# Kernel optimization log

Hardware: AMD Instinct MI355X
Metric: run time of the kernel (lower is better)

Reference implementation:

```python
import jax, jax.numpy as jnp
import numpy as np

EPS = 1e-5  # BatchNorm eps


def _conv(x, w, pad):
    # NCHW / OIHW stride-1 convolution (matches nn.Conv2d(..., padding=pad, bias=False))
    return jax.lax.conv_general_dilated(
        x, w, window_strides=(1, 1), padding=[(pad, pad), (pad, pad)],
        dimension_numbers=("NCHW", "OIHW", "NCHW"))


def _bn2d(x, g, b, m, v):
    # inference-mode BN folded to a per-channel affine
    s = g * jax.lax.rsqrt(v + EPS)
    return x * s[None, :, None, None] + (b - m * s)[None, :, None, None]


def _pool2(x):
    # AvgPool2d(2): non-overlapping 2x2 mean
    n, c, h, w = x.shape
    return x.reshape(n, c, h // 2, 2, w // 2, 2).mean(axis=(3, 5))


def _block(x, w, g, b, m, v):
    # Conv -> BN -> ReLU -> AvgPool2 -> Hardtanh(0,1)
    x = _conv(x, w, pad=2)
    x = _bn2d(x, g, b, m, v)
    x = jax.nn.relu(x)
    x = _pool2(x)
    return jnp.clip(x, 0.0, 1.0)


def setup_inputs() -> dict:
    key = jax.random.key(0)
    ks = jax.random.split(key, 24)
    B = 1024
    x = jax.random.uniform(ks[0], (B, 3, 32, 32), dtype=jnp.float32)

    def wgt(k, shape):
        fan_in = shape[1] * shape[2] * shape[3]
        return jax.random.normal(k, shape, jnp.float32) / np.float32(np.sqrt(fan_in))

    def bn(k, c):
        k1, k2, k3, k4 = jax.random.split(k, 4)
        g = jax.random.uniform(k1, (c,), jnp.float32, 0.5, 1.5)
        b = jax.random.normal(k2, (c,), jnp.float32) * 0.1
        m = jax.random.normal(k3, (c,), jnp.float32) * 0.1
        v = jax.random.uniform(k4, (c,), jnp.float32, 0.5, 1.5)
        return g, b, m, v

    w1 = wgt(ks[1], (32, 3, 5, 5))
    w2 = wgt(ks[2], (32, 32, 5, 5))
    w3 = wgt(ks[3], (64, 32, 5, 5))
    w4 = wgt(ks[4], (10, 64, 4, 4))  # fc1 as a 4x4 valid conv
    g1, b1, m1, v1 = bn(ks[5], 32)
    g2, b2, m2, v2 = bn(ks[6], 32)
    g3, b3, m3, v3 = bn(ks[7], 64)
    g4, b4, m4, v4 = bn(ks[8], 10)
    return dict(x=x,
                w1=w1, g1=g1, b1=b1, m1=m1, v1=v1,
                w2=w2, g2=g2, b2=b2, m2=m2, v2=v2,
                w3=w3, g3=g3, b3=b3, m3=m3, v3=v3,
                w4=w4, g4=g4, b4=b4, m4=m4, v4=v4)


def reference(x,
              w1, g1, b1, m1, v1,
              w2, g2, b2, m2, v2,
              w3, g3, b3, m3, v3,
              w4, g4, b4, m4, v4):
    x = _block(x, w1, g1, b1, m1, v1)   # [B,32,16,16]
    x = _block(x, w2, g2, b2, m2, v2)   # [B,32,8,8]
    x = _block(x, w3, g3, b3, m3, v3)   # [B,64,4,4]
    x = _conv(x, w4, pad=0)             # [B,10,1,1]
    x = x.reshape(x.shape[0], -1)       # flatten -> [B,10]
    s = g4 * jax.lax.rsqrt(v4 + EPS)    # BatchNorm1d_fixed (inference affine)
    return x * s[None, :] + (b4 - m4 * s)[None, :]
```

## Files before the change

kernel.cpp:

```cpp
#include <hip/hip_runtime.h>
#include <hip/hip_bf16.h>

#define EPS 1e-5f

typedef __bf16 v8bf __attribute__((ext_vector_type(8)));
typedef __bf16 v4bf __attribute__((ext_vector_type(4)));
typedef float  v4f  __attribute__((ext_vector_type(4)));

__global__ void k_wtrans(const float* __restrict__ w1, const float* __restrict__ w2,
                         const float* __restrict__ w3,
                         __hip_bfloat16* __restrict__ fb1, __hip_bfloat16* __restrict__ fb2,
                         __hip_bfloat16* __restrict__ fb3)
{
    int idx = blockIdx.x * 256 + threadIdx.x;
    if (idx < 640) {
        int lane = idx & 63, fi = idx >> 6;
        int ky = fi >> 1, nt = fi & 1;
        int oc = nt * 16 + (lane & 15), k0 = (lane >> 4) * 8;
        __hip_bfloat16* dst = fb1 + idx * 8;
        #pragma unroll
        for (int j = 0; j < 8; ++j) {
            int k = k0 + j, dx = k >> 2, ic = k & 3;
            float val = (dx < 5 && ic < 3) ? w1[oc * 75 + ic * 25 + ky * 5 + dx] : 0.f;
            dst[j] = __float2bfloat16(val);
        }
    } else if (idx < 640 + 3200) {
        int k2 = idx - 640;
        int lane = k2 & 63, fi = k2 >> 6;
        int tap = fi >> 1, nt = fi & 1;
        int oc = nt * 16 + (lane & 15), ic0 = (lane >> 4) * 8;
        __hip_bfloat16* dst = fb2 + k2 * 8;
        #pragma unroll
        for (int j = 0; j < 8; ++j)
            dst[j] = __float2bfloat16(w2[oc * 800 + (ic0 + j) * 25 + tap]);
    } else if (idx < 640 + 3200 + 6400) {
        int k3 = idx - 3840;
        int lane = k3 & 63, fi = k3 >> 6;
        int tap = fi >> 2, nt = fi & 3;
        int oc = nt * 16 + (lane & 15), ic0 = (lane >> 4) * 8;
        __hip_bfloat16* dst = fb3 + k3 * 8;
        #pragma unroll
        for (int j = 0; j < 8; ++j)
            dst[j] = __float2bfloat16(w3[oc * 800 + (ic0 + j) * 25 + tap]);
    }
}

#define XS2(row, col, blk) ((__hip_bfloat16*)(pool + (((((row)*20 + (col))*32) + (((blk) ^ ((col)&3))*8))*2)))
#define XS2S(row, col, oc) ((__hip_bfloat16*)(pool + (((((row)*20 + (col))*32) + ((((oc)>>3) ^ ((col)&3))*8) + ((oc)&7))*2)))
#define XS1(row, col)      ((__hip_bfloat16*)(pool + 25600 + ((((row)*39 + (col))*4)*2)))
#define XS3(row, col, blk) ((__hip_bfloat16*)(pool + 25600 + (((((row)*12 + (col))*32) + (((blk) ^ ((col)&3))*8))*2)))
#define XS3S(row, col, oc) ((__hip_bfloat16*)(pool + 25600 + (((((row)*12 + (col))*32) + ((((oc)>>3) ^ ((col)&3))*8) + ((oc)&7))*2)))

__global__ __launch_bounds__(512, 4) void k_fused(
    const float* __restrict__ x,
    const __hip_bfloat16* __restrict__ fb1,
    const __hip_bfloat16* __restrict__ fb2,
    const __hip_bfloat16* __restrict__ fb3,
    const float* __restrict__ w4,
    const float* __restrict__ g1, const float* __restrict__ b1,
    const float* __restrict__ m1, const float* __restrict__ v1,
    const float* __restrict__ g2, const float* __restrict__ b2,
    const float* __restrict__ m2, const float* __restrict__ v2,
    const float* __restrict__ g3, const float* __restrict__ b3,
    const float* __restrict__ m3, const float* __restrict__ v3,
    const float* __restrict__ g4, const float* __restrict__ b4,
    const float* __restrict__ m4, const float* __restrict__ v4,
    float* __restrict__ out)
{
    __shared__ __align__(16) unsigned char pool[36832];
    __shared__ float sc1[32], bi1[32], sc2[32], bi2[32], sc3[64], bi3[64];
    float* fin = (float*)pool;

    const int img = blockIdx.x, t = threadIdx.x;
    const int lane = t & 63, wave = t >> 6;
    const int lo = lane & 15, hi = lane >> 4;

    for (int i = t; i < 2302; i += 512) ((uint4*)pool)[i] = make_uint4(0, 0, 0, 0);
    if (t < 32) {
        float s = g1[t] * rsqrtf(v1[t] + EPS); sc1[t] = s; bi1[t] = b1[t] - m1[t] * s;
        float u = g2[t] * rsqrtf(v2[t] + EPS); sc2[t] = u; bi2[t] = b2[t] - m2[t] * u;
    }
    if (t < 64) {
        float s = g3[t] * rsqrtf(v3[t] + EPS); sc3[t] = s; bi3[t] = b3[t] - m3[t] * s;
    }
    __syncthreads();

    for (int i = t; i < 768; i += 512) {
        float4 val = *(const float4*)(x + (size_t)img * 3072 + i * 4);
        int ic = i >> 8, rem = i & 255;
        int y = rem >> 3, xx = (rem & 7) * 4;
        XS1(y + 2, xx + 2)[ic] = __float2bfloat16(val.x);
        XS1(y + 2, xx + 3)[ic] = __float2bfloat16(val.y);
        XS1(y + 2, xx + 4)[ic] = __float2bfloat16(val.z);
        XS1(y + 2, xx + 5)[ic] = __float2bfloat16(val.w);
    }
    __syncthreads();

    {
        const int y0 = 4 * wave;
        #pragma unroll
        for (int xh = 0; xh < 2; ++xh) {
            const int xx = xh * 16 + lo + hi * 2;
            v8bf av[8];
            #pragma unroll
            for (int r = 0; r < 8; ++r) {
                v4bf lo4 = *(const v4bf*)XS1(y0 + r, xx);
                v4bf hi4 = *(const v4bf*)XS1(y0 + r, xx + 1);
                av[r] = __builtin_shufflevector(lo4, hi4, 0, 1, 2, 3, 4, 5, 6, 7);
            }
            #pragma unroll
            for (int nt = 0; nt < 2; ++nt) {
                v8bf bw[5];
                #pragma unroll
                for (int ky = 0; ky < 5; ++ky)
                    bw[ky] = *(const v8bf*)(fb1 + ((ky * 2 + nt) * 64 + lane) * 8);
                v4f acc[2][2];
                #pragma unroll
                for (int a0 = 0; a0 < 2; ++a0)
                    #pragma unroll
                    for (int a1 = 0; a1 < 2; ++a1)
                        acc[a0][a1] = (v4f){0.f, 0.f, 0.f, 0.f};
                #pragma unroll
                for (int ky = 0; ky < 5; ++ky) {
                    acc[0][0] = __builtin_amdgcn_mfma_f32_16x16x32_bf16(av[ky],     bw[ky], acc[0][0], 0, 0, 0);
                    acc[0][1] = __builtin_amdgcn_mfma_f32_16x16x32_bf16(av[ky + 1], bw[ky], acc[0][1], 0, 0, 0);
                    acc[1][0] = __builtin_amdgcn_mfma_f32_16x16x32_bf16(av[ky + 2], bw[ky], acc[1][0], 0, 0, 0);
                    acc[1][1] = __builtin_amdgcn_mfma_f32_16x16x32_bf16(av[ky + 3], bw[ky], acc[1][1], 0, 0, 0);
                }
                const int oc = nt * 16 + lo;
                const float s = sc1[oc], bb = bi1[oc];
                #pragma unroll
                for (int pri = 0; pri < 2; ++pri) {
                    float u0 = fmaxf(fmaf(acc[pri][0][0], s, bb), 0.f);
                    float u1 = fmaxf(fmaf(acc[pri][0][1], s, bb), 0.f);
                    float u2 = fmaxf(fmaf(acc[pri][0][2], s, bb), 0.f);
                    float u3 = fmaxf(fmaf(acc[pri][0][3], s, bb), 0.f);
                    float q0 = fmaxf(fmaf(acc[pri][1][0], s, bb), 0.f);
                    float q1 = fmaxf(fmaf(acc[pri][1][1], s, bb), 0.f);
                    float q2 = fmaxf(fmaf(acc[pri][1][2], s, bb), 0.f);
                    float q3 = fmaxf(fmaf(acc[pri][1][3], s, bb), 0.f);
                    float p0 = fminf(0.25f * (u0 + u1 + q0 + q1), 1.f);
                    float p1 = fminf(0.25f * (u2 + u3 + q2 + q3), 1.f);
                    const int pr = 2 * wave + pri;
                    const int px = xh * 8 + hi * 2;
                    *XS2S(pr + 2, px + 2, oc) = __float2bfloat16(p0);
                    *XS2S(pr + 2, px + 3, oc) = __float2bfloat16(p1);
                }
            }
        }
    }
    __syncthreads();

    {
        uint* x3u = (uint*)(pool + 25600);
        for (int i = t; i < 1280; i += 512) {
            int u;
            if (i < 384)      u = i;
            else if (i < 768) u = 1920 + (i - 384);
            else {
                int j = i - 768;
                int r = 2 + (j >> 6), c = j & 63;
                u = r * 192 + (c < 32 ? c : 128 + c);
            }
            x3u[u] = 0u;
        }

        const int nt = wave & 1, wgrp = wave >> 1;
        v4f acc[2][2];
        #pragma unroll
        for (int a0 = 0; a0 < 2; ++a0)
            #pragma unroll
            for (int a1 = 0; a1 < 2; ++a1)
                acc[a0][a1] = (v4f){0.f, 0.f, 0.f, 0.f};

        #pragma unroll
        for (int kx = 0; kx < 5; ++kx) {
            v8bf bf[5];
            #pragma unroll
            for (int ky = 0; ky < 5; ++ky)
                bf[ky] = *(const v8bf*)(fb2 + ((ky * 5 + kx) * 2 + nt) * 512 + lane * 8);
            v8bf av[8];
            #pragma unroll
            for (int r = 0; r < 8; ++r)
                av[r] = *(const v8bf*)XS2(4 * wgrp + r, lo + kx, hi);
            #pragma unroll
            for (int ky = 0; ky < 5; ++ky) {
                acc[0][0] = __builtin_amdgcn_mfma_f32_16x16x32_bf16(av[ky],     bf[ky], acc[0][0], 0, 0, 0);
                acc[0][1] = __builtin_amdgcn_mfma_f32_16x16x32_bf16(av[ky + 1], bf[ky], acc[0][1], 0, 0, 0);
                acc[1][0] = __builtin_amdgcn_mfma_f32_16x16x32_bf16(av[ky + 2], bf[ky], acc[1][0], 0, 0, 0);
                acc[1][1] = __builtin_amdgcn_mfma_f32_16x16x32_bf16(av[ky + 3], bf[ky], acc[1][1], 0, 0, 0);
            }
        }

        const int oc = nt * 16 + lo;
        const float s = sc2[oc], bb = bi2[oc];
        #pragma unroll
        for (int pri = 0; pri < 2; ++pri) {
            const int rp = wgrp * 2 + pri;
            float u0 = fmaxf(fmaf(acc[pri][0][0], s, bb), 0.f);
            float u1 = fmaxf(fmaf(acc[pri][0][1], s, bb), 0.f);
            float u2 = fmaxf(fmaf(acc[pri][0][2], s, bb), 0.f);
            float u3 = fmaxf(fmaf(acc[pri][0][3], s, bb), 0.f);
            float q0 = fmaxf(fmaf(acc[pri][1][0], s, bb), 0.f);
            float q1 = fmaxf(fmaf(acc[pri][1][1], s, bb), 0.f);
            float q2 = fmaxf(fmaf(acc[pri][1][2], s, bb), 0.f);
            float q3 = fmaxf(fmaf(acc[pri][1][3], s, bb), 0.f);
            float p0 = fminf(0.25f * (u0 + u1 + q0 + q1), 1.f);
            float p1 = fminf(0.25f * (u2 + u3 + q2 + q3), 1.f);
            *XS3S(rp + 2, hi * 2 + 2, oc) = __float2bfloat16(p0);
            *XS3S(rp + 2, hi * 2 + 3, oc) = __float2bfloat16(p1);
        }
    }
    __syncthreads();

    {
        const int nt = wave >> 1, mh = wave & 1;
        const int oc = nt * 16 + lo;
        const int ya0 = lo >> 3, xa = lo & 7;
        v4f acc[2];
        #pragma unroll
        for (int q = 0; q < 2; ++q) acc[q] = (v4f){0.f, 0.f, 0.f, 0.f};

        #pragma unroll
        for (int ky = 0; ky < 5; ++ky) {
            v8bf bf[5];
            #pragma unroll
            for (int kx = 0; kx < 5; ++kx)
                bf[kx] = *(const v8bf*)(fb3 + ((ky * 5 + kx) * 4 + nt) * 512 + lane * 8);
            #pragma unroll
            for (int kx = 0; kx < 5; ++kx) {
                #pragma unroll
                for (int mi = 0; mi < 2; ++mi) {
                    const int mt = mh * 2 + mi;
                    v8bf av = *(const v8bf*)XS3(2 * mt + ya0 + ky, xa + kx, hi);
                    acc[mi] = __builtin_amdgcn_mfma_f32_16x16x32_bf16(av, bf[kx], acc[mi], 0, 0, 0);
                }
            }
        }

        const float s = sc3[oc], bb = bi3[oc];
        const int xb = (hi & 1) * 2;
        #pragma unroll
        for (int mi = 0; mi < 2; ++mi) {
            const int mt = mh * 2 + mi;
            float v0 = fmaxf(fmaf(acc[mi][0], s, bb), 0.f);
            float v1 = fmaxf(fmaf(acc[mi][1], s, bb), 0.f);
            float v2 = fmaxf(fmaf(acc[mi][2], s, bb), 0.f);
            float v3 = fmaxf(fmaf(acc[mi][3], s, bb), 0.f);
            float s01 = v0 + v1, s23 = v2 + v3;
            float o01 = __shfl_xor(s01, 32);
            float o23 = __shfl_xor(s23, 32);
            float p0 = fminf(0.25f * (s01 + o01), 1.f);
            float p1 = fminf(0.25f * (s23 + o23), 1.f);
            if (hi < 2) {
                fin[oc * 16 + mt * 4 + xb]     = p0;
                fin[oc * 16 + mt * 4 + xb + 1] = p1;
            }
        }
    }
    __syncthreads();

    {
        for (int oc = wave; oc < 10; oc += 8) {
            const float4* wp = (const float4*)(w4 + oc * 1024);
            const float4* fp = (const float4*)fin;
            float acc0 = 0.f, acc1 = 0.f;
            #pragma unroll
            for (int ch = 0; ch < 4; ++ch) {
                float4 a = fp[ch * 64 + lane];
                float4 w = wp[ch * 64 + lane];
                acc0 = fmaf(a.x, w.x, acc0); acc1 = fmaf(a.y, w.y, acc1);
                acc0 = fmaf(a.z, w.z, acc0); acc1 = fmaf(a.w, w.w, acc1);
            }
            float acc = acc0 + acc1;
            acc += __shfl_xor(acc, 1);
            acc += __shfl_xor(acc, 2);
            acc += __shfl_xor(acc, 4);
            acc += __shfl_xor(acc, 8);
            acc += __shfl_xor(acc, 16);
            acc += __shfl_xor(acc, 32);
            if (lane == 0) {
                float s = g4[oc] * rsqrtf(v4[oc] + EPS);
                out[img * 10 + oc] = acc * s + (b4[oc] - m4[oc] * s);
            }
        }
    }
}

extern "C" void kernel_launch(void* const* d_in, const int* in_sizes, int n_in,
                              void* d_out, int out_size, void* d_ws, size_t ws_size,
                              hipStream_t stream) {
    const float* x  = (const float*)d_in[0];
    const float* w1 = (const float*)d_in[1];
    const float* g1 = (const float*)d_in[2];
    const float* b1 = (const float*)d_in[3];
    const float* m1 = (const float*)d_in[4];
    const float* v1 = (const float*)d_in[5];
    const float* w2 = (const float*)d_in[6];
    const float* g2 = (const float*)d_in[7];
    const float* b2 = (const float*)d_in[8];
    const float* m2 = (const float*)d_in[9];
    const float* v2 = (const float*)d_in[10];
    const float* w3 = (const float*)d_in[11];
    const float* g3 = (const float*)d_in[12];
    const float* b3 = (const float*)d_in[13];
    const float* m3 = (const float*)d_in[14];
    const float* v3 = (const float*)d_in[15];
    const float* w4 = (const float*)d_in[16];
    const float* g4 = (const float*)d_in[17];
    const float* b4 = (const float*)d_in[18];
    const float* m4 = (const float*)d_in[19];
    const float* v4 = (const float*)d_in[20];
    float* out = (float*)d_out;

    char* base = (char*)d_ws;
    __hip_bfloat16* fb1 = (__hip_bfloat16*)base;
    __hip_bfloat16* fb2 = (__hip_bfloat16*)(base + 16384);
    __hip_bfloat16* fb3 = (__hip_bfloat16*)(base + 67584);

    k_wtrans<<<40, 256, 0, stream>>>(w1, w2, w3, fb1, fb2, fb3);
    k_fused<<<1024, 512, 0, stream>>>(x, fb1, fb2, fb3, w4,
                                      g1, b1, m1, v1, g2, b2, m2, v2,
                                      g3, b3, m3, v3, g4, b4, m4, v4, out);
}
```

Before: 40.00 us.

## Rework conv2/conv3 wave tiling, stronger LDS swizzle, border-only zeroing, packed input load

In conv2, each wave now owns one pooled output row and both output-channel tiles, so each A fragment feeds two MFMAs and fewer redundant A rows are loaded per wave. In conv3, each wave owns one M tile and two N tiles, loading A once per tap and streaming B directly. The LDS swizzle adds a second XOR term to reduce bank conflicts. Full LDS zeroing is replaced by zeroing only the padding borders, and the input is written as packed 3-channel bf16 cells with one barrier removed. The trade-off is more B-fragment registers in conv2 and more complex index arithmetic.

```diff
diff --git a/kernel.cpp b/kernel.cpp
--- a/kernel.cpp
+++ b/kernel.cpp
@@ -45,11 +45,12 @@
     }
 }
 
-#define XS2(row, col, blk) ((__hip_bfloat16*)(pool + (((((row)*20 + (col))*32) + (((blk) ^ ((col)&3))*8))*2)))
-#define XS2S(row, col, oc) ((__hip_bfloat16*)(pool + (((((row)*20 + (col))*32) + ((((oc)>>3) ^ ((col)&3))*8) + ((oc)&7))*2)))
+#define SWZ(blk, col)      ((blk) ^ ((col) & 3) ^ (((col) >> 2) & 3))
+#define XS2(row, col, blk) ((__hip_bfloat16*)(pool + (((((row)*20 + (col))*32) + (SWZ(blk,col)*8))*2)))
+#define XS2S(row, col, oc) ((__hip_bfloat16*)(pool + (((((row)*20 + (col))*32) + (SWZ((oc)>>3,col)*8) + ((oc)&7))*2)))
 #define XS1(row, col)      ((__hip_bfloat16*)(pool + 25600 + ((((row)*39 + (col))*4)*2)))
-#define XS3(row, col, blk) ((__hip_bfloat16*)(pool + 25600 + (((((row)*12 + (col))*32) + (((blk) ^ ((col)&3))*8))*2)))
-#define XS3S(row, col, oc) ((__hip_bfloat16*)(pool + 25600 + (((((row)*12 + (col))*32) + ((((oc)>>3) ^ ((col)&3))*8) + ((oc)&7))*2)))
+#define XS3(row, col, blk) ((__hip_bfloat16*)(pool + 25600 + (((((row)*12 + (col))*32) + (SWZ(blk,col)*8))*2)))
+#define XS3S(row, col, oc) ((__hip_bfloat16*)(pool + 25600 + (((((row)*12 + (col))*32) + (SWZ((oc)>>3,col)*8) + ((oc)&7))*2)))
 
 __global__ __launch_bounds__(512, 4) void k_fused(
     const float* __restrict__ x,
@@ -75,7 +76,6 @@
     const int lane = t & 63, wave = t >> 6;
     const int lo = lane & 15, hi = lane >> 4;
 
-    for (int i = t; i < 2302; i += 512) ((uint4*)pool)[i] = make_uint4(0, 0, 0, 0);
     if (t < 32) {
         float s = g1[t] * rsqrtf(v1[t] + EPS); sc1[t] = s; bi1[t] = b1[t] - m1[t] * s;
         float u = g2[t] * rsqrtf(v2[t] + EPS); sc2[t] = u; bi2[t] = b2[t] - m2[t] * u;
@@ -83,16 +83,31 @@
     if (t < 64) {
         float s = g3[t] * rsqrtf(v3[t] + EPS); sc3[t] = s; bi3[t] = b3[t] - m3[t] * s;
     }
-    __syncthreads();
-
-    for (int i = t; i < 768; i += 512) {
-        float4 val = *(const float4*)(x + (size_t)img * 3072 + i * 4);
-        int ic = i >> 8, rem = i & 255;
-        int y = rem >> 3, xx = (rem & 7) * 4;
-        XS1(y + 2, xx + 2)[ic] = __float2bfloat16(val.x);
-        XS1(y + 2, xx + 3)[ic] = __float2bfloat16(val.y);
-        XS1(y + 2, xx + 4)[ic] = __float2bfloat16(val.z);
-        XS1(y + 2, xx + 5)[ic] = __float2bfloat16(val.w);
+    for (int i = t; i < 956; i += 512) {
+        if (i < 380) {
+            int row, col;
+            if (i < 156) { int rr = i / 39; row = rr < 2 ? rr : rr + 32; col = i % 39; }
+            else { int j = i - 156; row = 2 + j / 7; int cc = j % 7; col = cc < 2 ? cc : cc + 32; }
+            *(uint2*)(pool + 25600 + (row * 39 + col) * 8) = make_uint2(0u, 0u);
+        } else {
+            int k = i - 380;
+            int cell = k >> 2, q = k & 3;
+            int row, col;
+            if (cell < 80) { int rr = cell / 20; row = rr < 2 ? rr : rr + 16; col = cell % 20; }
+            else { int j = cell - 80; row = 2 + (j >> 2); int c2 = j & 3; col = c2 < 2 ? c2 : c2 + 16; }
+            *(uint4*)(pool + ((row * 20 + col) * 32 + q * 8) * 2) = make_uint4(0u, 0u, 0u, 0u);
+        }
+    }
+    for (int c = t; c < 1024; c += 512) {
+        int y = c >> 5, xx = c & 31;
+        int base = img * 3072 + (y << 5) + xx;
+        float f0 = x[base], f1 = x[base + 1024], f2 = x[base + 2048];
+        __hip_bfloat16 h0 = __float2bfloat16(f0);
+        __hip_bfloat16 h1 = __float2bfloat16(f1);
+        __hip_bfloat16 h2 = __float2bfloat16(f2);
+        uint lo32 = (uint)*(unsigned short*)&h0 | ((uint)*(unsigned short*)&h1 << 16);
+        uint hi32 = (uint)*(unsigned short*)&h2;
+        *(uint2*)XS1(y + 2, xx + 2) = make_uint2(lo32, hi32);
     }
     __syncthreads();
 
@@ -165,7 +180,7 @@
             x3u[u] = 0u;
         }
 
-        const int nt = wave & 1, wgrp = wave >> 1;
+        const int rp = wave;
         v4f acc[2][2];
         #pragma unroll
         for (int a0 = 0; a0 < 2; ++a0)
@@ -175,36 +190,37 @@
 
         #pragma unroll
         for (int kx = 0; kx < 5; ++kx) {
-            v8bf bf[5];
+            v8bf bf[5][2];
             #pragma unroll
             for (int ky = 0; ky < 5; ++ky)
-                bf[ky] = *(const v8bf*)(fb2 + ((ky * 5 + kx) * 2 + nt) * 512 + lane * 8);
-            v8bf av[8];
-            #pragma unroll
-            for (int r = 0; r < 8; ++r)
-                av[r] = *(const v8bf*)XS2(4 * wgrp + r, lo + kx, hi);
+                #pragma unroll
+                for (int nt = 0; nt < 2; ++nt)
+                    bf[ky][nt] = *(const v8bf*)(fb2 + ((ky * 5 + kx) * 2 + nt) * 512 + lane * 8);
+            v8bf av[6];
+            #pragma unroll
+            for (int r = 0; r < 6; ++r)
+                av[r] = *(const v8bf*)XS2(2 * rp + r, lo + kx, hi);
             #pragma unroll
             for (int ky = 0; ky < 5; ++ky) {
-                acc[0][0] = __builtin_amdgcn_mfma_f32_16x16x32_bf16(av[ky],     bf[ky], acc[0][0], 0, 0, 0);
-                acc[0][1] = __builtin_amdgcn_mfma_f32_16x16x32_bf16(av[ky + 1], bf[ky], acc[0][1], 0, 0, 0);
-                acc[1][0] = __builtin_amdgcn_mfma_f32_16x16x32_bf16(av[ky + 2], bf[ky], acc[1][0], 0, 0, 0);
-                acc[1][1] = __builtin_amdgcn_mfma_f32_16x16x32_bf16(av[ky + 3], bf[ky], acc[1][1], 0, 0, 0);
-            }
-        }
-
-        const int oc = nt * 16 + lo;
-        const float s = sc2[oc], bb = bi2[oc];
-        #pragma unroll
-        for (int pri = 0; pri < 2; ++pri) {
-            const int rp = wgrp * 2 + pri;
-            float u0 = fmaxf(fmaf(acc[pri][0][0], s, bb), 0.f);
-            float u1 = fmaxf(fmaf(acc[pri][0][1], s, bb), 0.f);
-            float u2 = fmaxf(fmaf(acc[pri][0][2], s, bb), 0.f);
-            float u3 = fmaxf(fmaf(acc[pri][0][3], s, bb), 0.f);
-            float q0 = fmaxf(fmaf(acc[pri][1][0], s, bb), 0.f);
-            float q1 = fmaxf(fmaf(acc[pri][1][1], s, bb), 0.f);
-            float q2 = fmaxf(fmaf(acc[pri][1][2], s, bb), 0.f);
-            float q3 = fmaxf(fmaf(acc[pri][1][3], s, bb), 0.f);
+                acc[0][0] = __builtin_amdgcn_mfma_f32_16x16x32_bf16(av[ky],     bf[ky][0], acc[0][0], 0, 0, 0);
+                acc[0][1] = __builtin_amdgcn_mfma_f32_16x16x32_bf16(av[ky],     bf[ky][1], acc[0][1], 0, 0, 0);
+                acc[1][0] = __builtin_amdgcn_mfma_f32_16x16x32_bf16(av[ky + 1], bf[ky][0], acc[1][0], 0, 0, 0);
+                acc[1][1] = __builtin_amdgcn_mfma_f32_16x16x32_bf16(av[ky + 1], bf[ky][1], acc[1][1], 0, 0, 0);
+            }
+        }
+
+        #pragma unroll
+        for (int nt = 0; nt < 2; ++nt) {
+            const int oc = nt * 16 + lo;
+            const float s = sc2[oc], bb = bi2[oc];
+            float u0 = fmaxf(fmaf(acc[0][nt][0], s, bb), 0.f);
+            float u1 = fmaxf(fmaf(acc[0][nt][1], s, bb), 0.f);
+            float u2 = fmaxf(fmaf(acc[0][nt][2], s, bb), 0.f);
+            float u3 = fmaxf(fmaf(acc[0][nt][3], s, bb), 0.f);
+            float q0 = fmaxf(fmaf(acc[1][nt][0], s, bb), 0.f);
+            float q1 = fmaxf(fmaf(acc[1][nt][1], s, bb), 0.f);
+            float q2 = fmaxf(fmaf(acc[1][nt][2], s, bb), 0.f);
+            float q3 = fmaxf(fmaf(acc[1][nt][3], s, bb), 0.f);
             float p0 = fminf(0.25f * (u0 + u1 + q0 + q1), 1.f);
             float p1 = fminf(0.25f * (u2 + u3 + q2 + q3), 1.f);
             *XS3S(rp + 2, hi * 2 + 2, oc) = __float2bfloat16(p0);
@@ -214,39 +230,33 @@
     __syncthreads();
 
     {
-        const int nt = wave >> 1, mh = wave & 1;
-        const int oc = nt * 16 + lo;
+        const int mt = wave >> 1, nh = wave & 1;
         const int ya0 = lo >> 3, xa = lo & 7;
         v4f acc[2];
         #pragma unroll
         for (int q = 0; q < 2; ++q) acc[q] = (v4f){0.f, 0.f, 0.f, 0.f};
 
         #pragma unroll
-        for (int ky = 0; ky < 5; ++ky) {
-            v8bf bf[5];
-            #pragma unroll
-            for (int kx = 0; kx < 5; ++kx)
-                bf[kx] = *(const v8bf*)(fb3 + ((ky * 5 + kx) * 4 + nt) * 512 + lane * 8);
+        for (int ky = 0; ky < 5; ++ky)
             #pragma unroll
             for (int kx = 0; kx < 5; ++kx) {
-                #pragma unroll
-                for (int mi = 0; mi < 2; ++mi) {
-                    const int mt = mh * 2 + mi;
-                    v8bf av = *(const v8bf*)XS3(2 * mt + ya0 + ky, xa + kx, hi);
-                    acc[mi] = __builtin_amdgcn_mfma_f32_16x16x32_bf16(av, bf[kx], acc[mi], 0, 0, 0);
-                }
-            }
-        }
-
-        const float s = sc3[oc], bb = bi3[oc];
+                const int tap = ky * 5 + kx;
+                v8bf av = *(const v8bf*)XS3(2 * mt + ya0 + ky, xa + kx, hi);
+                v8bf b0 = *(const v8bf*)(fb3 + (tap * 4 + nh * 2 + 0) * 512 + lane * 8);
+                v8bf b1 = *(const v8bf*)(fb3 + (tap * 4 + nh * 2 + 1) * 512 + lane * 8);
+                acc[0] = __builtin_amdgcn_mfma_f32_16x16x32_bf16(av, b0, acc[0], 0, 0, 0);
+                acc[1] = __builtin_amdgcn_mfma_f32_16x16x32_bf16(av, b1, acc[1], 0, 0, 0);
+            }
+
         const int xb = (hi & 1) * 2;
         #pragma unroll
-        for (int mi = 0; mi < 2; ++mi) {
-            const int mt = mh * 2 + mi;
-            float v0 = fmaxf(fmaf(acc[mi][0], s, bb), 0.f);
-            float v1 = fmaxf(fmaf(acc[mi][1], s, bb), 0.f);
-            float v2 = fmaxf(fmaf(acc[mi][2], s, bb), 0.f);
-            float v3 = fmaxf(fmaf(acc[mi][3], s, bb), 0.f);
+        for (int ni = 0; ni < 2; ++ni) {
+            const int oc = (nh * 2 + ni) * 16 + lo;
+            const float s = sc3[oc], bb = bi3[oc];
+            float v0 = fmaxf(fmaf(acc[ni][0], s, bb), 0.f);
+            float v1 = fmaxf(fmaf(acc[ni][1], s, bb), 0.f);
+            float v2 = fmaxf(fmaf(acc[ni][2], s, bb), 0.f);
+            float v3 = fmaxf(fmaf(acc[ni][3], s, bb), 0.f);
             float s01 = v0 + v1, s23 = v2 + v3;
             float o01 = __shfl_xor(s01, 32);
             float o23 = __shfl_xor(s23, 32);
```

New measurement: 47.48 us. 18.7% more time.

## Process two images per block to reuse conv weight fragments

Applied to the files above, without the earlier changes.

Each workgroup now handles two images, with duplicated LDS buffers for both. Weight fragments loaded for conv1/conv2/conv3 are shared across the two images' MFMA sequences. Conv3's wave tiling is restructured so each wave covers two output-channel tiles for both images. This cuts global weight loads and per-block setup at the cost of doubled LDS, more accumulator registers and half as many blocks.

```diff
diff --git a/kernel.cpp b/kernel.cpp
--- a/kernel.cpp
+++ b/kernel.cpp
@@ -45,11 +45,12 @@
     }
 }
 
-#define XS2(row, col, blk) ((__hip_bfloat16*)(pool + (((((row)*20 + (col))*32) + (((blk) ^ ((col)&3))*8))*2)))
-#define XS2S(row, col, oc) ((__hip_bfloat16*)(pool + (((((row)*20 + (col))*32) + ((((oc)>>3) ^ ((col)&3))*8) + ((oc)&7))*2)))
-#define XS1(row, col)      ((__hip_bfloat16*)(pool + 25600 + ((((row)*39 + (col))*4)*2)))
-#define XS3(row, col, blk) ((__hip_bfloat16*)(pool + 25600 + (((((row)*12 + (col))*32) + (((blk) ^ ((col)&3))*8))*2)))
-#define XS3S(row, col, oc) ((__hip_bfloat16*)(pool + 25600 + (((((row)*12 + (col))*32) + ((((oc)>>3) ^ ((col)&3))*8) + ((oc)&7))*2)))
+#define SWZ(blk, col)          ((blk) ^ ((col) & 3))
+#define XS2(im, row, col, blk) ((__hip_bfloat16*)(pool + (im)*25600 + (((((row)*20 + (col))*32) + (SWZ(blk,col)*8))*2)))
+#define XS2S(im, row, col, oc) ((__hip_bfloat16*)(pool + (im)*25600 + (((((row)*20 + (col))*32) + (SWZ((oc)>>3,col)*8) + ((oc)&7))*2)))
+#define XS1(im, row, col)      ((__hip_bfloat16*)(pool + 51200 + (im)*11232 + ((((row)*39 + (col))*4)*2)))
+#define XS3(im, row, col, blk) ((__hip_bfloat16*)(pool + 51200 + (im)*9216 + (((((row)*12 + (col))*32) + (SWZ(blk,col)*8))*2)))
+#define XS3S(im, row, col, oc) ((__hip_bfloat16*)(pool + 51200 + (im)*9216 + (((((row)*12 + (col))*32) + (SWZ((oc)>>3,col)*8) + ((oc)&7))*2)))
 
 __global__ __launch_bounds__(512, 4) void k_fused(
     const float* __restrict__ x,
@@ -67,15 +68,14 @@
     const float* __restrict__ m4, const float* __restrict__ v4,
     float* __restrict__ out)
 {
-    __shared__ __align__(16) unsigned char pool[36832];
+    __shared__ __align__(16) unsigned char pool[73664];
     __shared__ float sc1[32], bi1[32], sc2[32], bi2[32], sc3[64], bi3[64];
-    float* fin = (float*)pool;
-
-    const int img = blockIdx.x, t = threadIdx.x;
+
+    const int img0 = blockIdx.x * 2, t = threadIdx.x;
     const int lane = t & 63, wave = t >> 6;
     const int lo = lane & 15, hi = lane >> 4;
 
-    for (int i = t; i < 2302; i += 512) ((uint4*)pool)[i] = make_uint4(0, 0, 0, 0);
+    for (int i = t; i < 4604; i += 512) ((uint4*)pool)[i] = make_uint4(0, 0, 0, 0);
     if (t < 32) {
         float s = g1[t] * rsqrtf(v1[t] + EPS); sc1[t] = s; bi1[t] = b1[t] - m1[t] * s;
         float u = g2[t] * rsqrtf(v2[t] + EPS); sc2[t] = u; bi2[t] = b2[t] - m2[t] * u;
@@ -85,66 +85,75 @@
     }
     __syncthreads();
 
-    for (int i = t; i < 768; i += 512) {
-        float4 val = *(const float4*)(x + (size_t)img * 3072 + i * 4);
-        int ic = i >> 8, rem = i & 255;
-        int y = rem >> 3, xx = (rem & 7) * 4;
-        XS1(y + 2, xx + 2)[ic] = __float2bfloat16(val.x);
-        XS1(y + 2, xx + 3)[ic] = __float2bfloat16(val.y);
-        XS1(y + 2, xx + 4)[ic] = __float2bfloat16(val.z);
-        XS1(y + 2, xx + 5)[ic] = __float2bfloat16(val.w);
+    #pragma unroll
+    for (int im = 0; im < 2; ++im) {
+        for (int i = t; i < 768; i += 512) {
+            float4 val = *(const float4*)(x + (size_t)(img0 + im) * 3072 + i * 4);
+            int ic = i >> 8, rem = i & 255;
+            int y = rem >> 3, xx = (rem & 7) * 4;
+            XS1(im, y + 2, xx + 2)[ic] = __float2bfloat16(val.x);
+            XS1(im, y + 2, xx + 3)[ic] = __float2bfloat16(val.y);
+            XS1(im, y + 2, xx + 4)[ic] = __float2bfloat16(val.z);
+            XS1(im, y + 2, xx + 5)[ic] = __float2bfloat16(val.w);
+        }
     }
     __syncthreads();
 
     {
+        v8bf bw[5][2];
+        #pragma unroll
+        for (int ky = 0; ky < 5; ++ky)
+            #pragma unroll
+            for (int nt = 0; nt < 2; ++nt)
+                bw[ky][nt] = *(const v8bf*)(fb1 + ((ky * 2 + nt) * 64 + lane) * 8);
+
         const int y0 = 4 * wave;
         #pragma unroll
-        for (int xh = 0; xh < 2; ++xh) {
-            const int xx = xh * 16 + lo + hi * 2;
-            v8bf av[8];
-            #pragma unroll
-            for (int r = 0; r < 8; ++r) {
-                v4bf lo4 = *(const v4bf*)XS1(y0 + r, xx);
-                v4bf hi4 = *(const v4bf*)XS1(y0 + r, xx + 1);
-                av[r] = __builtin_shufflevector(lo4, hi4, 0, 1, 2, 3, 4, 5, 6, 7);
-            }
-            #pragma unroll
-            for (int nt = 0; nt < 2; ++nt) {
-                v8bf bw[5];
-                #pragma unroll
-                for (int ky = 0; ky < 5; ++ky)
-                    bw[ky] = *(const v8bf*)(fb1 + ((ky * 2 + nt) * 64 + lane) * 8);
-                v4f acc[2][2];
-                #pragma unroll
-                for (int a0 = 0; a0 < 2; ++a0)
+        for (int im = 0; im < 2; ++im) {
+            #pragma unroll
+            for (int xh = 0; xh < 2; ++xh) {
+                const int xx = xh * 16 + lo + hi * 2;
+                v8bf av[8];
+                #pragma unroll
+                for (int r = 0; r < 8; ++r) {
+                    v4bf lo4 = *(const v4bf*)XS1(im, y0 + r, xx);
+                    v4bf hi4 = *(const v4bf*)XS1(im, y0 + r, xx + 1);
+                    av[r] = __builtin_shufflevector(lo4, hi4, 0, 1, 2, 3, 4, 5, 6, 7);
+                }
+                #pragma unroll
+                for (int nt = 0; nt < 2; ++nt) {
+                    v4f acc[2][2];
                     #pragma unroll
-                    for (int a1 = 0; a1 < 2; ++a1)
-                        acc[a0][a1] = (v4f){0.f, 0.f, 0.f, 0.f};
-                #pragma unroll
-                for (int ky = 0; ky < 5; ++ky) {
-                    acc[0][0] = __builtin_amdgcn_mfma_f32_16x16x32_bf16(av[ky],     bw[ky], acc[0][0], 0, 0, 0);
-                    acc[0][1] = __builtin_amdgcn_mfma_f32_16x16x32_bf16(av[ky + 1], bw[ky], acc[0][1], 0, 0, 0);
-                    acc[1][0] = __builtin_amdgcn_mfma_f32_16x16x32_bf16(av[ky + 2], bw[ky], acc[1][0], 0, 0, 0);
-                    acc[1][1] = __builtin_amdgcn_mfma_f32_16x16x32_bf16(av[ky + 3], bw[ky], acc[1][1], 0, 0, 0);
-                }
-                const int oc = nt * 16 + lo;
-                const float s = sc1[oc], bb = bi1[oc];
-                #pragma unroll
-                for (int pri = 0; pri < 2; ++pri) {
-                    float u0 = fmaxf(fmaf(acc[pri][0][0], s, bb), 0.f);
-                    float u1 = fmaxf(fmaf(acc[pri][0][1], s, bb), 0.f);
-                    float u2 = fmaxf(fmaf(acc[pri][0][2], s, bb), 0.f);
-                    float u3 = fmaxf(fmaf(acc[pri][0][3], s, bb), 0.f);
-                    float q0 = fmaxf(fmaf(acc[pri][1][0], s, bb), 0.f);
-                    float q1 = fmaxf(fmaf(acc[pri][1][1], s, bb), 0.f);
-                    float q2 = fmaxf(fmaf(acc[pri][1][2], s, bb), 0.f);
-                    float q3 = fmaxf(fmaf(acc[pri][1][3], s, bb), 0.f);
-                    float p0 = fminf(0.25f * (u0 + u1 + q0 + q1), 1.f);
-                    float p1 = fminf(0.25f * (u2 + u3 + q2 + q3), 1.f);
-                    const int pr = 2 * wave + pri;
-                    const int px = xh * 8 + hi * 2;
-                    *XS2S(pr + 2, px + 2, oc) = __float2bfloat16(p0);
-                    *XS2S(pr + 2, px + 3, oc) = __float2bfloat16(p1);
+                    for (int a0 = 0; a0 < 2; ++a0)
+                        #pragma unroll
+                        for (int a1 = 0; a1 < 2; ++a1)
+                            acc[a0][a1] = (v4f){0.f, 0.f, 0.f, 0.f};
+                    #pragma unroll
+                    for (int ky = 0; ky < 5; ++ky) {
+                        acc[0][0] = __builtin_amdgcn_mfma_f32_16x16x32_bf16(av[ky],     bw[ky][nt], acc[0][0], 0, 0, 0);
+                        acc[0][1] = __builtin_amdgcn_mfma_f32_16x16x32_bf16(av[ky + 1], bw[ky][nt], acc[0][1], 0, 0, 0);
+                        acc[1][0] = __builtin_amdgcn_mfma_f32_16x16x32_bf16(av[ky + 2], bw[ky][nt], acc[1][0], 0, 0, 0);
+                        acc[1][1] = __builtin_amdgcn_mfma_f32_16x16x32_bf16(av[ky + 3], bw[ky][nt], acc[1][1], 0, 0, 0);
+                    }
+                    const int oc = nt * 16 + lo;
+                    const float s = sc1[oc], bb = bi1[oc];
+                    #pragma unroll
+                    for (int pri = 0; pri < 2; ++pri) {
+                        float u0 = fmaxf(fmaf(acc[pri][0][0], s, bb), 0.f);
+                        float u1 = fmaxf(fmaf(acc[pri][0][1], s, bb), 0.f);
+                        float u2 = fmaxf(fmaf(acc[pri][0][2], s, bb), 0.f);
+                        float u3 = fmaxf(fmaf(acc[pri][0][3], s, bb), 0.f);
+                        float q0 = fmaxf(fmaf(acc[pri][1][0], s, bb), 0.f);
+                        float q1 = fmaxf(fmaf(acc[pri][1][1], s, bb), 0.f);
+                        float q2 = fmaxf(fmaf(acc[pri][1][2], s, bb), 0.f);
+                        float q3 = fmaxf(fmaf(acc[pri][1][3], s, bb), 0.f);
+                        float p0 = fminf(0.25f * (u0 + u1 + q0 + q1), 1.f);
+                        float p1 = fminf(0.25f * (u2 + u3 + q2 + q3), 1.f);
+                        const int pr = 2 * wave + pri;
+                        const int px = xh * 8 + hi * 2;
+                        *XS2S(im, pr + 2, px + 2, oc) = __float2bfloat16(p0);
+                        *XS2S(im, pr + 2, px + 3, oc) = __float2bfloat16(p1);
+                    }
                 }
             }
         }
@@ -152,26 +161,29 @@
     __syncthreads();
 
     {
-        uint* x3u = (uint*)(pool + 25600);
-        for (int i = t; i < 1280; i += 512) {
+        for (int i = t; i < 2560; i += 512) {
+            int im = i >= 1280, j = i - im * 1280;
+            uint* x3u = (uint*)(pool + 51200 + im * 9216);
             int u;
-            if (i < 384)      u = i;
-            else if (i < 768) u = 1920 + (i - 384);
+            if (j < 384)      u = j;
+            else if (j < 768) u = 1920 + (j - 384);
             else {
-                int j = i - 768;
-                int r = 2 + (j >> 6), c = j & 63;
+                int k = j - 768;
+                int r = 2 + (k >> 6), c = k & 63;
                 u = r * 192 + (c < 32 ? c : 128 + c);
             }
             x3u[u] = 0u;
         }
 
         const int nt = wave & 1, wgrp = wave >> 1;
-        v4f acc[2][2];
+        v4f acc2[2][2][2];
         #pragma unroll
         for (int a0 = 0; a0 < 2; ++a0)
             #pragma unroll
             for (int a1 = 0; a1 < 2; ++a1)
-                acc[a0][a1] = (v4f){0.f, 0.f, 0.f, 0.f};
+                #pragma unroll
+                for (int a2 = 0; a2 < 2; ++a2)
+                    acc2[a0][a1][a2] = (v4f){0.f, 0.f, 0.f, 0.f};
 
         #pragma unroll
         for (int kx = 0; kx < 5; ++kx) {
@@ -179,91 +191,101 @@
             #pragma unroll
             for (int ky = 0; ky < 5; ++ky)
                 bf[ky] = *(const v8bf*)(fb2 + ((ky * 5 + kx) * 2 + nt) * 512 + lane * 8);
-            v8bf av[8];
-            #pragma unroll
-            for (int r = 0; r < 8; ++r)
-                av[r] = *(const v8bf*)XS2(4 * wgrp + r, lo + kx, hi);
-            #pragma unroll
-            for (int ky = 0; ky < 5; ++ky) {
-                acc[0][0] = __builtin_amdgcn_mfma_f32_16x16x32_bf16(av[ky],     bf[ky], acc[0][0], 0, 0, 0);
-                acc[0][1] = __builtin_amdgcn_mfma_f32_16x16x32_bf16(av[ky + 1], bf[ky], acc[0][1], 0, 0, 0);
-                acc[1][0] = __builtin_amdgcn_mfma_f32_16x16x32_bf16(av[ky + 2], bf[ky], acc[1][0], 0, 0, 0);
-                acc[1][1] = __builtin_amdgcn_mfma_f32_16x16x32_bf16(av[ky + 3], bf[ky], acc[1][1], 0, 0, 0);
+            #pragma unroll
+            for (int im = 0; im < 2; ++im) {
+                v8bf av[8];
+                #pragma unroll
+                for (int r = 0; r < 8; ++r)
+                    av[r] = *(const v8bf*)XS2(im, 4 * wgrp + r, lo + kx, hi);
+                #pragma unroll
+                for (int ky = 0; ky < 5; ++ky) {
+                    acc2[im][0][0] = __builtin_amdgcn_mfma_f32_16x16x32_bf16(av[ky],     bf[ky], acc2[im][0][0], 0, 0, 0);
+                    acc2[im][0][1] = __builtin_amdgcn_mfma_f32_16x16x32_bf16(av[ky + 1], bf[ky], acc2[im][0][1], 0, 0, 0);
+                    acc2[im][1][0] = __builtin_amdgcn_mfma_f32_16x16x32_bf16(av[ky + 2], bf[ky], acc2[im][1][0], 0, 0, 0);
+                    acc2[im][1][1] = __builtin_amdgcn_mfma_f32_16x16x32_bf16(av[ky + 3], bf[ky], acc2[im][1][1], 0, 0, 0);
+                }
             }
         }
 
         const int oc = nt * 16 + lo;
         const float s = sc2[oc], bb = bi2[oc];
         #pragma unroll
-        for (int pri = 0; pri < 2; ++pri) {
-            const int rp = wgrp * 2 + pri;
-            float u0 = fmaxf(fmaf(acc[pri][0][0], s, bb), 0.f);
-            float u1 = fmaxf(fmaf(acc[pri][0][1], s, bb), 0.f);
-            float u2 = fmaxf(fmaf(acc[pri][0][2], s, bb), 0.f);
-            float u3 = fmaxf(fmaf(acc[pri][0][3], s, bb), 0.f);
-            float q0 = fmaxf(fmaf(acc[pri][1][0], s, bb), 0.f);
-            float q1 = fmaxf(fmaf(acc[pri][1][1], s, bb), 0.f);
-            float q2 = fmaxf(fmaf(acc[pri][1][2], s, bb), 0.f);
-            float q3 = fmaxf(fmaf(acc[pri][1][3], s, bb), 0.f);
-            float p0 = fminf(0.25f * (u0 + u1 + q0 + q1), 1.f);
-            float p1 = fminf(0.25f * (u2 + u3 + q2 + q3), 1.f);
-            *XS3S(rp + 2, hi * 2 + 2, oc) = __float2bfloat16(p0);
-            *XS3S(rp + 2, hi * 2 + 3, oc) = __float2bfloat16(p1);
-        }
+        for (int im = 0; im < 2; ++im)
+            #pragma unroll
+            for (int pri = 0; pri < 2; ++pri) {
+                const int rp = wgrp * 2 + pri;
+                float u0 = fmaxf(fmaf(acc2[im][pri][0][0], s, bb), 0.f);
+                float u1 = fmaxf(fmaf(acc2[im][pri][0][1], s, bb), 0.f);
+                float u2 = fmaxf(fmaf(acc2[im][pri][0][2], s, bb), 0.f);
+                float u3 = fmaxf(fmaf(acc2[im][pri][0][3], s, bb), 0.f);
+                float q0 = fmaxf(fmaf(acc2[im][pri][1][0], s, bb), 0.f);
+                float q1 = fmaxf(fmaf(acc2[im][pri][1][1], s, bb), 0.f);
+                float q2 = fmaxf(fmaf(acc2[im][pri][1][2], s, bb), 0.f);
+                float q3 = fmaxf(fmaf(acc2[im][pri][1][3], s, bb), 0.f);
+                float p0 = fminf(0.25f * (u0 + u1 + q0 + q1), 1.f);
+                float p1 = fminf(0.25f * (u2 + u3 + q2 + q3), 1.f);
+                *XS3S(im, rp + 2, hi * 2 + 2, oc) = __float2bfloat16(p0);
+                *XS3S(im, rp + 2, hi * 2 + 3, oc) = __float2bfloat16(p1);
+            }
     }
     __syncthreads();
 
     {
-        const int nt = wave >> 1, mh = wave & 1;
-        const int oc = nt * 16 + lo;
+        const int mt = wave >> 1, nh = wave & 1;
         const int ya0 = lo >> 3, xa = lo & 7;
-        v4f acc[2];
-        #pragma unroll
-        for (int q = 0; q < 2; ++q) acc[q] = (v4f){0.f, 0.f, 0.f, 0.f};
-
-        #pragma unroll
-        for (int ky = 0; ky < 5; ++ky) {
-            v8bf bf[5];
-            #pragma unroll
-            for (int kx = 0; kx < 5; ++kx)
-                bf[kx] = *(const v8bf*)(fb3 + ((ky * 5 + kx) * 4 + nt) * 512 + lane * 8);
+        v4f acc3[2][2];
+        #pragma unroll
+        for (int a0 = 0; a0 < 2; ++a0)
+            #pragma unroll
+            for (int a1 = 0; a1 < 2; ++a1)
+                acc3[a0][a1] = (v4f){0.f, 0.f, 0.f, 0.f};
+
+        #pragma unroll
+        for (int ky = 0; ky < 5; ++ky)
             #pragma unroll
             for (int kx = 0; kx < 5; ++kx) {
-                #pragma unroll
-                for (int mi = 0; mi < 2; ++mi) {
-                    const int mt = mh * 2 + mi;
-                    v8bf av = *(const v8bf*)XS3(2 * mt + ya0 + ky, xa + kx, hi);
-                    acc[mi] = __builtin_amdgcn_mfma_f32_16x16x32_bf16(av, bf[kx], acc[mi], 0, 0, 0);
-                }
-            }
-        }
-
-        const float s = sc3[oc], bb = bi3[oc];
+                const int tap = ky * 5 + kx;
+                v8bf b0 = *(const v8bf*)(fb3 + (tap * 4 + nh * 2 + 0) * 512 + lane * 8);
+                v8bf b1 = *(const v8bf*)(fb3 + (tap * 4 + nh * 2 + 1) * 512 + lane * 8);
+                #pragma unroll
+                for (int im = 0; im < 2; ++im) {
+                    v8bf av = *(const v8bf*)XS3(im, 2 * mt + ya0 + ky, xa + kx, hi);
+                    acc3[im][0] = __builtin_amdgcn_mfma_f32_16x16x32_bf16(av, b0, acc3[im][0], 0, 0, 0);
+                    acc3[im][1] = __builtin_amdgcn_mfma_f32_16x16x32_bf16(av, b1, acc3[im][1], 0, 0, 0);
+                }
+            }
+
         const int xb = (hi & 1) * 2;
         #pragma unroll
-        for (int mi = 0; mi < 2; ++mi) {
-            const int mt = mh * 2 + mi;
-            float v0 = fmaxf(fmaf(acc[mi][0], s, bb), 0.f);
-            float v1 = fmaxf(fmaf(acc[mi][1], s, bb), 0.f);
-            float v2 = fmaxf(fmaf(acc[mi][2], s, bb), 0.f);
-            float v3 = fmaxf(fmaf(acc[mi][3], s, bb), 0.f);
-            float s01 = v0 + v1, s23 = v2 + v3;
-            float o01 = __shfl_xor(s01, 32);
-            float o23 = __shfl_xor(s23, 32);
-            float p0 = fminf(0.25f * (s01 + o01), 1.f);
-            float p1 = fminf(0.25f * (s23 + o23), 1.f);
-            if (hi < 2) {
-                fin[oc * 16 + mt * 4 + xb]     = p0;
-                fin[oc * 16 + mt * 4 + xb + 1] = p1;
+        for (int im = 0; im < 2; ++im) {
+            float* fin = (float*)(pool + im * 4096);
+            #pragma unroll
+            for (int ni = 0; ni < 2; ++ni) {
+                const int oc = (nh * 2 + ni) * 16 + lo;
+                const float s = sc3[oc], bb = bi3[oc];
+                float v0 = fmaxf(fmaf(acc3[im][ni][0], s, bb), 0.f);
+                float v1 = fmaxf(fmaf(acc3[im][ni][1], s, bb), 0.f);
+                float v2 = fmaxf(fmaf(acc3[im][ni][2], s, bb), 0.f);
+                float v3 = fmaxf(fmaf(acc3[im][ni][3], s, bb), 0.f);
+                float s01 = v0 + v1, s23 = v2 + v3;
+                float o01 = __shfl_xor(s01, 32);
+                float o23 = __shfl_xor(s23, 32);
+                float p0 = fminf(0.25f * (s01 + o01), 1.f);
+                float p1 = fminf(0.25f * (s23 + o23), 1.f);
+                if (hi < 2) {
+                    fin[oc * 16 + mt * 4 + xb]     = p0;
+                    fin[oc * 16 + mt * 4 + xb + 1] = p1;
+                }
             }
         }
     }
     __syncthreads();
 
     {
-        for (int oc = wave; oc < 10; oc += 8) {
+        for (int task = wave; task < 20; task += 8) {
+            const int im = task >= 10, oc = task - im * 10;
             const float4* wp = (const float4*)(w4 + oc * 1024);
-            const float4* fp = (const float4*)fin;
+            const float4* fp = (const float4*)(pool + im * 4096);
             float acc0 = 0.f, acc1 = 0.f;
             #pragma unroll
             for (int ch = 0; ch < 4; ++ch) {
@@ -281,7 +303,7 @@
             acc += __shfl_xor(acc, 32);
             if (lane == 0) {
                 float s = g4[oc] * rsqrtf(v4[oc] + EPS);
-                out[img * 10 + oc] = acc * s + (b4[oc] - m4[oc] * s);
+                out[(img0 + im) * 10 + oc] = acc * s + (b4[oc] - m4[oc] * s);
             }
         }
     }
@@ -319,7 +341,7 @@
     __hip_bfloat16* fb3 = (__hip_bfloat16*)(base + 67584);
 
     k_wtrans<<<40, 256, 0, stream>>>(w1, w2, w3, fb1, fb2, fb3);
-    k_fused<<<1024, 512, 0, stream>>>(x, fb1, fb2, fb3, w4,
-                                      g1, b1, m1, v1, g2, b2, m2, v2,
-                                      g3, b3, m3, v3, g4, b4, m4, v4, out);
+    k_fused<<<512, 512, 0, stream>>>(x, fb1, fb2, fb3, w4,
+                                     g1, b1, m1, v1, g2, b2, m2, v2,
+                                     g3, b3, m3, v3, g4, b4, m4, v4, out);
 }
```

After: 39.36 us. Within noise of the previous version (-1.6%).
